# Performance work log

Hardware: AMD Instinct MI355X
Metric: run time of the kernel (lower is better)

Reference implementation:

```python
import jax, jax.numpy as jnp
import numpy as np

B, N, M, HW = 8, 256, 32, 32768
W_CLASS, W_CENTER, W_MASK, W_DICE = 2.0, 1.0, 5.0, 2.0


def setup_inputs() -> dict:
    key = jax.random.key(0)
    ks = jax.random.split(key, 6)
    sem_cls_prob = jax.random.uniform(ks[0], (B, N, 1), dtype=jnp.float32)
    center_dist = jax.random.uniform(ks[1], (B, N, M), dtype=jnp.float32)
    mask_heatmaps = jax.random.normal(ks[2], (B, HW, N), dtype=jnp.float32)
    # binary targets, as assumed by the dice/BCE cost math
    mask_tgt = jnp.round(jax.random.uniform(ks[3], (B, M, HW), dtype=jnp.float32))
    gt_plane_sem_cls_label = jax.random.randint(ks[4], (B, M), 0, 2).astype(jnp.int64)
    nactual_gt = jax.random.randint(ks[5], (B,), 1, M + 1).astype(jnp.int64)
    return {
        'sem_cls_prob': sem_cls_prob,
        'center_dist': center_dist,
        'mask_heatmaps': mask_heatmaps,
        'mask_tgt': mask_tgt,
        'gt_plane_sem_cls_label': gt_plane_sem_cls_label,
        'nactual_gt': nactual_gt,
    }


def _final_cost(sem_cls_prob, center_dist, mask_heatmaps, mask_tgt, labels):
    # class cost: -gathered prob from cat(1-p, p) -> [B, N, M]
    cls_cat = jnp.concatenate([1.0 - sem_cls_prob, sem_cls_prob], axis=-1)  # [B, N, 2]
    lbl = jnp.broadcast_to(labels[:, None, :], (B, N, M))
    class_mat = -jnp.take_along_axis(cls_cat, lbl, axis=2)

    x = jnp.swapaxes(mask_heatmaps, 1, 2)  # [B, N, HW] logits (mask_heatmaps[b].T)
    # BCE-with-logits: pos = softplus(-x) (target=1), neg = x + softplus(-x) (target=0)
    pos = jax.nn.softplus(-x)
    neg = x + pos
    cost_mask = (jnp.einsum('bnc,bmc->bnm', pos, mask_tgt)
                 + jnp.einsum('bnc,bmc->bnm', neg, 1.0 - mask_tgt)) / HW

    s = jax.nn.sigmoid(x)
    numerator = 2.0 * jnp.einsum('bnc,bmc->bnm', s, mask_tgt)
    denominator = s.sum(-1)[:, :, None] + mask_tgt.sum(-1)[:, None, :]
    cost_dice = 1.0 - (numerator + 1.0) / (denominator + 1.0)

    return (W_CLASS * class_mat + W_CENTER * center_dist
            + W_MASK * cost_mask + W_DICE * cost_dice)


def reference(sem_cls_prob, center_dist, mask_heatmaps, mask_tgt,
              gt_plane_sem_cls_label, nactual_gt):
    # nactual_gt only gates the (serial, CPU) Hungarian step, which is out of
    # kernel scope; the GPU-side math is the fused final cost matrix.
    return _final_cost(sem_cls_prob, center_dist, mask_heatmaps, mask_tgt,
                       gt_plane_sem_cls_label)
```

## Files before the change

### kernel.cpp

```cpp
#include <hip/hip_runtime.h>
#include <hip/hip_bf16.h>

#define NB   8
#define NN   256
#define NM   32
#define NHW  32768

#define CCH    64
#define CSLAB  (NHW / CCH)
#define KC     32
#define KSTEPS (CSLAB / KC)

#define OFF_DXP  0
#define SZ_DXP   (CCH*NB*NN*NM)
#define OFF_DSP  (OFF_DXP + SZ_DXP)
#define OFF_SNP  (OFF_DSP + SZ_DXP)
#define SZ_SNP   (CCH*NB*NN)
#define OFF_SSP  (OFF_SNP + SZ_SNP)
#define OFF_STGT (OFF_SSP + SZ_SNP)

typedef _Float16 half8 __attribute__((ext_vector_type(8)));
typedef float    f32x4 __attribute__((ext_vector_type(4)));

#define MFMA16(a, b, c) __builtin_amdgcn_mfma_f32_16x16x32_f16(a, b, c, 0, 0, 0)

typedef const __attribute__((address_space(1))) unsigned int* gp_t;
typedef __attribute__((address_space(3))) unsigned int*       lp_t;

__device__ __forceinline__ void stage_row(const float* gsrc, float* ldst,
                                          int lane, int rot) {
    const int src = ((lane << 2) - rot) & 255;
#if __has_builtin(__builtin_amdgcn_global_load_lds)
    __builtin_amdgcn_global_load_lds((gp_t)(const void*)(gsrc + src),
                                     (lp_t)(void*)ldst, 16, 0, 0);
#else
    float4 v = *(const float4*)(gsrc + src);
    *(float4*)(ldst + lane * 4) = v;
#endif
}

__global__ __launch_bounds__(512, 4) void cost_main(
    const float* __restrict__ X,
    const float* __restrict__ T,
    float* __restrict__ ws) {
    const int blk = blockIdx.x;
    const int b   = blk & 7;
    const int ch  = blk >> 3;

    const int tid  = threadIdx.x;
    const int wave = tid >> 6;
    const int lane = tid & 63;
    const int l16  = lane & 15;
    const int quad = lane >> 4;

    const int c0 = ch * CSLAB;

    __shared__ __align__(16) float xs[2][KC][NN];

    const float* Xbase = X + ((size_t)b * NHW + c0) * NN;
    const float* Tp0   = T + ((size_t)b * NM + l16) * NHW + c0 + quad * 8;
    const float* Tp1   = Tp0 + (size_t)16 * NHW;

    const int col0 = ((wave << 5) + l16 + (quad << 3)) & 255;
    const int col1 = (col0 + 16) & 255;

#pragma unroll
    for (int r = 0; r < 4; ++r) {
        const int row = wave + r * 8;
        stage_row(Xbase + (size_t)row * NN, &xs[0][row][0], lane, r << 3);
    }

    f32x4 ax0[2], ax1[2], as0[2], as1[2];
#pragma unroll
    for (int f = 0; f < 2; ++f) {
        ax0[f] = f32x4{0.f, 0.f, 0.f, 0.f};
        ax1[f] = f32x4{0.f, 0.f, 0.f, 0.f};
        as0[f] = f32x4{0.f, 0.f, 0.f, 0.f};
        as1[f] = f32x4{0.f, 0.f, 0.f, 0.f};
    }
    float sneg[2] = {0.f, 0.f};
    float ssig[2] = {0.f, 0.f};
    float ts0 = 0.f, ts1 = 0.f;

    for (int ks = 0; ks < KSTEPS; ++ks) {
        __syncthreads();
        const int nb = ks + 1;
        if (nb < KSTEPS) {
            const float* Xn = Xbase + (size_t)nb * KC * NN;
#pragma unroll
            for (int r = 0; r < 4; ++r) {
                const int row = wave + r * 8;
                stage_row(Xn + (size_t)row * NN, &xs[nb & 1][row][0], lane, r << 3);
            }
        }

        float4 ta = *(const float4*)(Tp0 + ks * KC);
        float4 tb = *(const float4*)(Tp0 + ks * KC + 4);
        float4 tc = *(const float4*)(Tp1 + ks * KC);
        float4 td = *(const float4*)(Tp1 + ks * KC + 4);
        half8 ht0 = {(_Float16)ta.x, (_Float16)ta.y, (_Float16)ta.z, (_Float16)ta.w,
                     (_Float16)tb.x, (_Float16)tb.y, (_Float16)tb.z, (_Float16)tb.w};
        half8 ht1 = {(_Float16)tc.x, (_Float16)tc.y, (_Float16)tc.z, (_Float16)tc.w,
                     (_Float16)td.x, (_Float16)td.y, (_Float16)td.z, (_Float16)td.w};
        ts0 += (ta.x + ta.y) + (ta.z + ta.w) + (tb.x + tb.y) + (tb.z + tb.w);
        ts1 += (tc.x + tc.y) + (tc.z + tc.w) + (td.x + td.y) + (td.z + td.w);

#pragma unroll
        for (int f = 0; f < 2; ++f) {
            const int colf = f ? col1 : col0;
            float xv[8];
#pragma unroll
            for (int j = 0; j < 8; ++j)
                xv[j] = xs[ks & 1][quad * 8 + j][colf];
            half8 hx, hs;
#pragma unroll
            for (int j = 0; j < 8; ++j) {
                float x = xv[j];
                float e = __expf(-fabsf(x));
                float rc = __builtin_amdgcn_rcpf(1.f + e);
                float s  = (x >= 0.f) ? rc : 1.f - rc;
                float pos = fmaxf(-x, 0.f) + __logf(1.f + e);
                sneg[f] += x + pos;
                ssig[f] += s;
                hx[j] = (_Float16)x;
                hs[j] = (_Float16)s;
            }
            ax0[f] = MFMA16(hx, ht0, ax0[f]);
            ax1[f] = MFMA16(hx, ht1, ax1[f]);
            as0[f] = MFMA16(hs, ht0, as0[f]);
            as1[f] = MFMA16(hs, ht1, as1[f]);
        }
    }

#pragma unroll
    for (int f = 0; f < 2; ++f) {
        float sn = sneg[f], ss = ssig[f];
        sn += __shfl_xor(sn, 16); sn += __shfl_xor(sn, 32);
        ss += __shfl_xor(ss, 16); ss += __shfl_xor(ss, 32);
        if (lane < 16) {
            const size_t sb = ((size_t)ch * NB + b) * NN + wave * 32 + f * 16 + l16;
            ws[OFF_SNP + sb] = sn;
            ws[OFF_SSP + sb] = ss;
        }
    }
    if (wave == 0) {
        float t0 = ts0, t1 = ts1;
        t0 += __shfl_xor(t0, 16); t0 += __shfl_xor(t0, 32);
        t1 += __shfl_xor(t1, 16); t1 += __shfl_xor(t1, 32);
        if (lane < 16) {
            const size_t tb_ = ((size_t)ch * NB + b) * NM;
            ws[OFF_STGT + tb_ + l16]      = t0;
            ws[OFF_STGT + tb_ + l16 + 16] = t1;
        }
    }
    const size_t dbase = ((size_t)ch * NB + b) * NN * NM;
#pragma unroll
    for (int f = 0; f < 2; ++f) {
#pragma unroll
        for (int r = 0; r < 4; ++r) {
            const int n = wave * 32 + f * 16 + quad * 4 + r;
            const size_t o = dbase + (size_t)n * NM;
            ws[OFF_DXP + o + l16]      = ax0[f][r];
            ws[OFF_DXP + o + l16 + 16] = ax1[f][r];
            ws[OFF_DSP + o + l16]      = as0[f][r];
            ws[OFF_DSP + o + l16 + 16] = as1[f][r];
        }
    }
}

__global__ __launch_bounds__(256) void cost_finalize(
    const float* __restrict__ P,
    const float* __restrict__ CD,
    const int*   __restrict__ LAB,
    const float* __restrict__ ws,
    float* __restrict__ out) {
    const int bn = blockIdx.x;
    const int n  = bn & 255;
    const int b  = bn >> 8;
    const int t  = threadIdx.x;
    const int m  = t & 31;
    const int q  = t >> 5;

    float dx = 0.f, ds = 0.f, sn = 0.f, ss = 0.f, st = 0.f;
#pragma unroll
    for (int k = 0; k < 8; ++k) {
        const int ch = q * 8 + k;
        const size_t e = (size_t)ch * NB + b;
        const size_t o = (e * NN + n) * NM + m;
        dx += ws[OFF_DXP + o];
        ds += ws[OFF_DSP + o];
        sn += ws[OFF_SNP + e * NN + n];
        ss += ws[OFF_SSP + e * NN + n];
        st += ws[OFF_STGT + e * NM + m];
    }

    __shared__ float red[5][8][32];
    red[0][q][m] = dx; red[1][q][m] = ds; red[2][q][m] = sn;
    red[3][q][m] = ss; red[4][q][m] = st;
    __syncthreads();

    if (t < 32) {
        float a0 = 0.f, a1 = 0.f, a2 = 0.f, a3 = 0.f, a4 = 0.f;
#pragma unroll
        for (int k = 0; k < 8; ++k) {
            a0 += red[0][k][m]; a1 += red[1][k][m]; a2 += red[2][k][m];
            a3 += red[3][k][m]; a4 += red[4][k][m];
        }
        const float p   = P[bn];
        const int   lab = LAB[b * NM + m];
        const float cls = lab ? -p : (p - 1.f);

        const float cmask = (a2 - a0) * (1.f / (float)NHW);
        const float dice  = 1.f - (2.f * a1 + 1.f) / (a3 + a4 + 1.f);

        const size_t o = (size_t)bn * NM + m;
        out[o] = 2.f * cls + CD[o] + 5.f * cmask + 2.f * dice;
    }
}

extern "C" void kernel_launch(void* const* d_in, const int* in_sizes, int n_in,
                              void* d_out, int out_size, void* d_ws, size_t ws_size,
                              hipStream_t stream) {
    const float* P   = (const float*)d_in[0];
    const float* CD  = (const float*)d_in[1];
    const float* X   = (const float*)d_in[2];
    const float* T   = (const float*)d_in[3];
    const int*   LAB = (const int*)d_in[4];
    float* out = (float*)d_out;
    float* ws  = (float*)d_ws;

    hipLaunchKernelGGL(cost_main, dim3(NB * CCH), dim3(512), 0, stream, X, T, ws);
    hipLaunchKernelGGL(cost_finalize, dim3(NB * NN), dim3(256), 0, stream,
                       P, CD, LAB, ws, out);
}
```

Before: 420.8 us.

## Replace LDS staging with direct register double-buffered loads and split N across blocks

The main kernel no longer stages X tiles into shared memory through global_load_lds with barriers. Each lane now loads its eight X values per fragment straight from global memory into registers, using a two-set software pipeline that overlaps the next step's loads with the current compute. Blocks shrink to 256 threads and the N dimension is split into two halves, doubling the grid. The aim is to remove LDS traffic and __syncthreads stalls, at the cost of narrow scalar global loads (16 lanes per 64-byte row segment), redundant T loads across the two halves, and higher register pressure.

```diff
diff --git a/kernel.cpp b/kernel.cpp
--- a/kernel.cpp
+++ b/kernel.cpp
@@ -1,5 +1,4 @@
 #include <hip/hip_runtime.h>
-#include <hip/hip_bf16.h>
 
 #define NB   8
 #define NN   256
@@ -24,28 +23,33 @@
 
 #define MFMA16(a, b, c) __builtin_amdgcn_mfma_f32_16x16x32_f16(a, b, c, 0, 0, 0)
 
-typedef const __attribute__((address_space(1))) unsigned int* gp_t;
-typedef __attribute__((address_space(3))) unsigned int*       lp_t;
-
-__device__ __forceinline__ void stage_row(const float* gsrc, float* ldst,
-                                          int lane, int rot) {
-    const int src = ((lane << 2) - rot) & 255;
-#if __has_builtin(__builtin_amdgcn_global_load_lds)
-    __builtin_amdgcn_global_load_lds((gp_t)(const void*)(gsrc + src),
-                                     (lp_t)(void*)ldst, 16, 0, 0);
-#else
-    float4 v = *(const float4*)(gsrc + src);
-    *(float4*)(ldst + lane * 4) = v;
-#endif
-}
-
-__global__ __launch_bounds__(512, 4) void cost_main(
+struct Set {
+    float  xa[8], xb[8];
+    float4 ta, tb, tc, td;
+};
+
+__device__ __forceinline__ void load_set(Set& s, const float* Xk,
+                                         const float* Tq0, const float* Tq1) {
+    s.ta = *(const float4*)(Tq0);
+    s.tb = *(const float4*)(Tq0 + 4);
+    s.tc = *(const float4*)(Tq1);
+    s.td = *(const float4*)(Tq1 + 4);
+#pragma unroll
+    for (int j = 0; j < 8; ++j) {
+        s.xa[j] = Xk[j * NN];
+        s.xb[j] = Xk[j * NN + 16];
+    }
+}
+
+__global__ __launch_bounds__(256, 4) void cost_main(
     const float* __restrict__ X,
     const float* __restrict__ T,
     float* __restrict__ ws) {
-    const int blk = blockIdx.x;
-    const int b   = blk & 7;
-    const int ch  = blk >> 3;
+    const int blk  = blockIdx.x;
+    const int b    = blk & 7;
+    const int r_   = blk >> 3;
+    const int ch   = r_ >> 1;
+    const int half = r_ & 1;
 
     const int tid  = threadIdx.x;
     const int wave = tid >> 6;
@@ -54,21 +58,11 @@
     const int quad = lane >> 4;
 
     const int c0 = ch * CSLAB;
-
-    __shared__ __align__(16) float xs[2][KC][NN];
-
-    const float* Xbase = X + ((size_t)b * NHW + c0) * NN;
-    const float* Tp0   = T + ((size_t)b * NM + l16) * NHW + c0 + quad * 8;
-    const float* Tp1   = Tp0 + (size_t)16 * NHW;
-
-    const int col0 = ((wave << 5) + l16 + (quad << 3)) & 255;
-    const int col1 = (col0 + 16) & 255;
-
-#pragma unroll
-    for (int r = 0; r < 4; ++r) {
-        const int row = wave + r * 8;
-        stage_row(Xbase + (size_t)row * NN, &xs[0][row][0], lane, r << 3);
-    }
+    const int n0 = half * 128 + wave * 32;
+
+    const float* Xp  = X + ((size_t)(b * NHW + c0 + quad * 8)) * NN + n0 + l16;
+    const float* Tq0 = T + ((size_t)b * NM + l16) * NHW + c0 + quad * 8;
+    const float* Tq1 = Tq0 + (size_t)16 * NHW;
 
     f32x4 ax0[2], ax1[2], as0[2], as1[2];
 #pragma unroll
@@ -82,54 +76,47 @@
     float ssig[2] = {0.f, 0.f};
     float ts0 = 0.f, ts1 = 0.f;
 
-    for (int ks = 0; ks < KSTEPS; ++ks) {
-        __syncthreads();
-        const int nb = ks + 1;
-        if (nb < KSTEPS) {
-            const float* Xn = Xbase + (size_t)nb * KC * NN;
-#pragma unroll
-            for (int r = 0; r < 4; ++r) {
-                const int row = wave + r * 8;
-                stage_row(Xn + (size_t)row * NN, &xs[nb & 1][row][0], lane, r << 3);
-            }
-        }
-
-        float4 ta = *(const float4*)(Tp0 + ks * KC);
-        float4 tb = *(const float4*)(Tp0 + ks * KC + 4);
-        float4 tc = *(const float4*)(Tp1 + ks * KC);
-        float4 td = *(const float4*)(Tp1 + ks * KC + 4);
-        half8 ht0 = {(_Float16)ta.x, (_Float16)ta.y, (_Float16)ta.z, (_Float16)ta.w,
-                     (_Float16)tb.x, (_Float16)tb.y, (_Float16)tb.z, (_Float16)tb.w};
-        half8 ht1 = {(_Float16)tc.x, (_Float16)tc.y, (_Float16)tc.z, (_Float16)tc.w,
-                     (_Float16)td.x, (_Float16)td.y, (_Float16)td.z, (_Float16)td.w};
-        ts0 += (ta.x + ta.y) + (ta.z + ta.w) + (tb.x + tb.y) + (tb.z + tb.w);
-        ts1 += (tc.x + tc.y) + (tc.z + tc.w) + (td.x + td.y) + (td.z + td.w);
-
+    auto compute = [&](const Set& s) {
+        half8 ht0 = {(_Float16)s.ta.x, (_Float16)s.ta.y, (_Float16)s.ta.z, (_Float16)s.ta.w,
+                     (_Float16)s.tb.x, (_Float16)s.tb.y, (_Float16)s.tb.z, (_Float16)s.tb.w};
+        half8 ht1 = {(_Float16)s.tc.x, (_Float16)s.tc.y, (_Float16)s.tc.z, (_Float16)s.tc.w,
+                     (_Float16)s.td.x, (_Float16)s.td.y, (_Float16)s.td.z, (_Float16)s.td.w};
+        ts0 += (s.ta.x + s.ta.y) + (s.ta.z + s.ta.w) + (s.tb.x + s.tb.y) + (s.tb.z + s.tb.w);
+        ts1 += (s.tc.x + s.tc.y) + (s.tc.z + s.tc.w) + (s.td.x + s.td.y) + (s.td.z + s.td.w);
 #pragma unroll
         for (int f = 0; f < 2; ++f) {
-            const int colf = f ? col1 : col0;
-            float xv[8];
-#pragma unroll
-            for (int j = 0; j < 8; ++j)
-                xv[j] = xs[ks & 1][quad * 8 + j][colf];
             half8 hx, hs;
 #pragma unroll
             for (int j = 0; j < 8; ++j) {
-                float x = xv[j];
-                float e = __expf(-fabsf(x));
+                float x  = f ? s.xb[j] : s.xa[j];
+                float e  = __expf(-fabsf(x));
                 float rc = __builtin_amdgcn_rcpf(1.f + e);
-                float s  = (x >= 0.f) ? rc : 1.f - rc;
+                float sg = (x >= 0.f) ? rc : 1.f - rc;
                 float pos = fmaxf(-x, 0.f) + __logf(1.f + e);
                 sneg[f] += x + pos;
-                ssig[f] += s;
+                ssig[f] += sg;
                 hx[j] = (_Float16)x;
-                hs[j] = (_Float16)s;
+                hs[j] = (_Float16)sg;
             }
             ax0[f] = MFMA16(hx, ht0, ax0[f]);
             ax1[f] = MFMA16(hx, ht1, ax1[f]);
             as0[f] = MFMA16(hs, ht0, as0[f]);
             as1[f] = MFMA16(hs, ht1, as1[f]);
         }
+    };
+
+    Set A, B;
+    load_set(A, Xp, Tq0, Tq1);
+#pragma unroll 1
+    for (int it = 0; it < KSTEPS / 2; ++it) {
+        const int ko = 2 * it + 1;
+        load_set(B, Xp + (size_t)ko * KC * NN, Tq0 + ko * KC, Tq1 + ko * KC);
+        compute(A);
+        if (it + 1 < KSTEPS / 2) {
+            const int kn = 2 * it + 2;
+            load_set(A, Xp + (size_t)kn * KC * NN, Tq0 + kn * KC, Tq1 + kn * KC);
+        }
+        compute(B);
     }
 
 #pragma unroll
@@ -138,12 +125,12 @@
         sn += __shfl_xor(sn, 16); sn += __shfl_xor(sn, 32);
         ss += __shfl_xor(ss, 16); ss += __shfl_xor(ss, 32);
         if (lane < 16) {
-            const size_t sb = ((size_t)ch * NB + b) * NN + wave * 32 + f * 16 + l16;
+            const size_t sb = ((size_t)ch * NB + b) * NN + n0 + f * 16 + l16;
             ws[OFF_SNP + sb] = sn;
             ws[OFF_SSP + sb] = ss;
         }
     }
-    if (wave == 0) {
+    if (wave == 0 && half == 0) {
         float t0 = ts0, t1 = ts1;
         t0 += __shfl_xor(t0, 16); t0 += __shfl_xor(t0, 32);
         t1 += __shfl_xor(t1, 16); t1 += __shfl_xor(t1, 32);
@@ -158,7 +145,7 @@
     for (int f = 0; f < 2; ++f) {
 #pragma unroll
         for (int r = 0; r < 4; ++r) {
-            const int n = wave * 32 + f * 16 + quad * 4 + r;
+            const int n = n0 + f * 16 + quad * 4 + r;
             const size_t o = dbase + (size_t)n * NM;
             ws[OFF_DXP + o + l16]      = ax0[f][r];
             ws[OFF_DXP + o + l16 + 16] = ax1[f][r];
@@ -229,7 +216,7 @@
     float* out = (float*)d_out;
     float* ws  = (float*)d_ws;
 
-    hipLaunchKernelGGL(cost_main, dim3(NB * CCH), dim3(512), 0, stream, X, T, ws);
+    hipLaunchKernelGGL(cost_main, dim3(NB * CCH * 2), dim3(256), 0, stream, X, T, ws);
     hipLaunchKernelGGL(cost_finalize, dim3(NB * NN), dim3(256), 0, stream,
                        P, CD, LAB, ws, out);
 }
```

Result: slower. 586.4 us (+39.3%).
